# Optimization experiments

Hardware: AMD Instinct MI355X
Metric: run time of the kernel (lower is better)

The kernel has to match this reference:

```python
import math
import jax, jax.numpy as jnp
import numpy as np

NH, NKV, HD = 16, 8, 128  # n_heads, n_kv_heads, head_dim from config

def setup_inputs() -> dict:
    key = jax.random.key(0)
    ks = jax.random.split(key, 5)
    B, T, D = 2, 2048, 2048
    KV = NKV * HD  # 1024
    s = 1.0 / math.sqrt(D)
    return {
        "x": jax.random.normal(ks[0], (B, T, D), dtype=jnp.float32),
        "Wq": jax.random.normal(ks[1], (D, D), dtype=jnp.float32) * s,
        "Wk": jax.random.normal(ks[2], (KV, D), dtype=jnp.float32) * s,
        "Wv": jax.random.normal(ks[3], (KV, D), dtype=jnp.float32) * s,
        "Wo": jax.random.normal(ks[4], (D, D), dtype=jnp.float32) * s,
    }

def reference(x, Wq, Wk, Wv, Wo):
    B, T, D = x.shape
    groups = NH // NKV
    scale = 1.0 / math.sqrt(HD)
    # Projections (torch Linear: y = x @ W.T)
    q = (x @ Wq.T).reshape(B, T, NH, HD).transpose(0, 2, 1, 3)    # [B, nh, T, hd]
    k = (x @ Wk.T).reshape(B, T, NKV, HD).transpose(0, 2, 1, 3)   # [B, nkv, T, hd]
    v = (x @ Wv.T).reshape(B, T, NKV, HD).transpose(0, 2, 1, 3)   # [B, nkv, T, hd]
    kv_state = jnp.concatenate([k, v], axis=-1)                    # [B, nkv, T, 2*hd]
    # GQA: replicate kv heads (repeat_interleave along head dim)
    k = jnp.repeat(k, groups, axis=1)                              # [B, nh, T, hd]
    v = jnp.repeat(v, groups, axis=1)
    scores = jnp.einsum('bhqd,bhkd->bhqk', q, k) * scale           # [B, nh, T, T]
    causal = jnp.tril(jnp.ones((T, T), dtype=bool))
    scores = jnp.where(causal, scores, jnp.finfo(scores.dtype).min)
    probs = jax.nn.softmax(scores, axis=-1)
    attn = jnp.einsum('bhqk,bhkd->bhqd', probs, v)                 # [B, nh, T, hd]
    attn = attn.transpose(0, 2, 1, 3).reshape(B, T, NH * HD)
    output = attn @ Wo.T
    return (output, kv_state)
```

## Files before the change

kernel.cpp:

```cpp
#include <hip/hip_runtime.h>
#include <hip/hip_bf16.h>
#include <cstdint>
#include <cstddef>

#define DEV __device__ __forceinline__

typedef __attribute__((ext_vector_type(8))) short short8;
typedef __attribute__((ext_vector_type(4))) float f32x4;
typedef __attribute__((ext_vector_type(8))) __bf16 bf16x8;

DEV unsigned short f2bf(float f) {
    unsigned u = __builtin_bit_cast(unsigned, f);
    u += 0x7fffu + ((u >> 16) & 1u);
    return (unsigned short)(u >> 16);
}

DEV unsigned short f2bf_hw(float f) {
    return __builtin_bit_cast(unsigned short, (__bf16)f);
}

DEV f32x4 mfma16(short8 a, short8 b, f32x4 c) {
    return __builtin_amdgcn_mfma_f32_16x16x32_bf16(
        __builtin_bit_cast(bf16x8, a), __builtin_bit_cast(bf16x8, b), c, 0, 0, 0);
}

#define GLD_TO_LDS16(g, l)                                                  \
    __builtin_amdgcn_global_load_lds(                                       \
        (const __attribute__((address_space(1))) void*)(g),                 \
        (__attribute__((address_space(3))) void*)(l), 16, 0, 0)

__global__ void cvt_all(const float* __restrict__ x,  const float* __restrict__ wq,
                        const float* __restrict__ wk, const float* __restrict__ wv,
                        const float* __restrict__ wo,
                        unsigned short* __restrict__ xb,  unsigned short* __restrict__ wqb,
                        unsigned short* __restrict__ wkb, unsigned short* __restrict__ wvb,
                        unsigned short* __restrict__ wob) {
    constexpr int NX = 1048576, NQ = 524288, NK = 262144, NV = 262144, NO = 524288;
    constexpr int C1 = NX, C2 = C1 + NQ, C3 = C2 + NK, C4 = C3 + NV, C5 = C4 + NO;
    int i = blockIdx.x * blockDim.x + threadIdx.x;
    int stride = gridDim.x * blockDim.x;
    for (; i < C5; i += stride) {
        const float* s;
        unsigned short* d;
        int j;
        if (i < C1)      { s = x;  d = xb;  j = i; }
        else if (i < C2) { s = wq; d = wqb; j = i - C1; }
        else if (i < C3) { s = wk; d = wkb; j = i - C2; }
        else if (i < C4) { s = wv; d = wvb; j = i - C3; }
        else             { s = wo; d = wob; j = i - C4; }
        const f32x4* sp = (const f32x4*)(s + (size_t)j * 8);
        f32x4 a = sp[0], bq = sp[1];
        short8 o;
        o[0] = (short)f2bf(a[0]);  o[1] = (short)f2bf(a[1]);
        o[2] = (short)f2bf(a[2]);  o[3] = (short)f2bf(a[3]);
        o[4] = (short)f2bf(bq[0]); o[5] = (short)f2bf(bq[1]);
        o[6] = (short)f2bf(bq[2]); o[7] = (short)f2bf(bq[3]);
        *(short8*)(d + (size_t)j * 8) = o;
    }
}

__global__ __launch_bounds__(256) void transpose_v(
    const unsigned short* __restrict__ src, unsigned short* __restrict__ dst) {
    __shared__ __align__(16) unsigned short tile[64 * 64];
    const int t0 = blockIdx.x * 64;
    const int d0 = blockIdx.y * 64;
    const int b  = blockIdx.z;
    const int tid = threadIdx.x;
#pragma unroll
    for (int p = 0; p < 2; ++p) {
        int ch = tid + p * 256;
        int it = ch >> 3, ic8 = ch & 7;
        short8 v = *(const short8*)(src + (size_t)(b * 2048 + t0 + it) * 1024 + d0 + ic8 * 8);
        *(short8*)&tile[it * 64 + ((ic8 ^ (it & 7)) << 3)] = v;
    }
    __syncthreads();
#pragma unroll
    for (int p = 0; p < 2; ++p) {
        int ch = tid + p * 256;
        int od = ch >> 3, ot8 = ch & 7;
        short8 v;
#pragma unroll
        for (int j = 0; j < 8; ++j) {
            int t = ot8 * 8 + j;
            v[j] = (short)tile[t * 64 + ((((od >> 3) ^ (t & 7)) << 3) | (od & 7))];
        }
        *(short8*)(dst + (size_t)(b * 1024 + d0 + od) * 2048 + t0 + ot8 * 8) = v;
    }
}

__global__ __launch_bounds__(512, 2) void gemm_qkv_8p(
    const unsigned short* __restrict__ A,
    const unsigned short* __restrict__ Wq, const unsigned short* __restrict__ Wk,
    const unsigned short* __restrict__ Wv,
    unsigned short* __restrict__ Qo, unsigned short* __restrict__ Ko,
    unsigned short* __restrict__ Vo, float* __restrict__ kvf) {
    constexpr int K = 2048, BM = 256, KT = K / 64;
    __shared__ __align__(16) unsigned short sA[2][2][BM][32];
    __shared__ __align__(16) unsigned short sB[2][2][BM][32];

    const int tid = threadIdx.x, lane = tid & 63, w = tid >> 6;
    const int wm = w >> 2, wn = w & 3;
    const int lrow = lane & 15, lg = lane >> 4;
    const int m0 = blockIdx.y * BM, n0 = blockIdx.x * BM;

    const unsigned short* Bp;
    unsigned short* Co;
    int c0, ostr, doff = 0;
    bool iskv = false;
    if (n0 < 2048)      { Bp = Wq + (size_t)n0 * K;        Co = Qo; c0 = n0;        ostr = 2048; }
    else if (n0 < 3072) { Bp = Wk + (size_t)(n0-2048) * K; Co = Ko; c0 = n0 - 2048; ostr = 1024; iskv = true; }
    else                { Bp = Wv + (size_t)(n0-3072) * K; Co = Vo; c0 = n0 - 3072; ostr = 1024; iskv = true; doff = 128; }

    const unsigned short* Ab = A + (size_t)m0 * K;

    auto stage = [&](const unsigned short* gcol, unsigned short* lds) {
#pragma unroll
        for (int p = 0; p < 2; ++p) {
            int ch = tid + p * 512;
            int row = ch >> 2;
            int slot = (ch & 3) ^ (row & 3);
            GLD_TO_LDS16(gcol + (size_t)row * K + slot * 8, lds + ch * 8);
        }
    };

    f32x4 acc[8][4];
#pragma unroll
    for (int i = 0; i < 8; ++i)
#pragma unroll
        for (int j = 0; j < 4; ++j) acc[i][j] = (f32x4)0.f;

    const int xoff = (lg * 8) ^ ((lrow & 3) << 3);
    const int arow0 = wm * 128 + lrow;
    const int brow0 = wn * 64 + lrow;
    short8 afrag[4], bfrag[4];

    stage(Ab,      &sA[0][0][0][0]);
    stage(Bp,      &sB[0][0][0][0]);
    stage(Ab + 32, &sA[0][1][0][0]);
    stage(Bp + 32, &sB[0][1][0][0]);
    asm volatile("s_waitcnt vmcnt(4)\n\ts_barrier" ::: "memory");

#define PHASE(BUF, NB, KS, MQ, DOSTAGE, VM)                                        \
    do {                                                                           \
        if ((MQ) == 0) {                                                           \
            _Pragma("unroll")                                                      \
            for (int ni = 0; ni < 4; ++ni)                                         \
                bfrag[ni] = *(const short8*)(&sB[BUF][KS][brow0 + ni * 16][0] + xoff); \
        }                                                                          \
        _Pragma("unroll")                                                          \
        for (int mi = 0; mi < 4; ++mi)                                             \
            afrag[mi] = *(const short8*)(&sA[BUF][KS][arow0 + (MQ) * 64 + mi * 16][0] + xoff); \
        if (DOSTAGE) {                                                             \
            if ((MQ) == 0) stage(An + (KS) * 32, &sA[NB][KS][0][0]);               \
            else           stage(Bn + (KS) * 32, &sB[NB][KS][0][0]);               \
        }                                                                          \
        asm volatile("s_barrier" ::: "memory");                                    \
        asm volatile("s_waitcnt lgkmcnt(0)" ::: "memory");                         \
        __builtin_amdgcn_sched_barrier(0);                                         \
        __builtin_amdgcn_s_setprio(1);                                             \
        _Pragma("unroll")                                                          \
        for (int mi = 0; mi < 4; ++mi)                                             \
            _Pragma("unroll")                                                      \
            for (int ni = 0; ni < 4; ++ni)                                         \
                acc[(MQ) * 4 + mi][ni] = mfma16(afrag[mi], bfrag[ni], acc[(MQ) * 4 + mi][ni]); \
        __builtin_amdgcn_s_setprio(0);                                             \
        if ((VM) == 4)      asm volatile("s_waitcnt vmcnt(4)" ::: "memory");       \
        else if ((VM) == 0) asm volatile("s_waitcnt vmcnt(0)" ::: "memory");       \
        asm volatile("s_barrier" ::: "memory");                                    \
    } while (0)

    for (int kt = 0; kt < KT; ++kt) {
        const int buf = kt & 1, nb = buf ^ 1;
        const bool pre = (kt + 1 < KT);
        const unsigned short* An = Ab + (kt + 1) * 64;
        const unsigned short* Bn = Bp + (kt + 1) * 64;
        PHASE(buf, nb, 0, 0, pre, -1);
        PHASE(buf, nb, 0, 1, pre, pre ? 4 : 0);
        PHASE(buf, nb, 1, 0, pre, -1);
        PHASE(buf, nb, 1, 1, pre, pre ? 4 : -1);
    }
#undef PHASE

    const int lrow4 = (lane >> 4) * 4, lcol = lane & 15;
#pragma unroll
    for (int mi = 0; mi < 8; ++mi) {
#pragma unroll
        for (int ni = 0; ni < 4; ++ni) {
#pragma unroll
            for (int r = 0; r < 4; ++r) {
                int row = m0 + wm * 128 + mi * 16 + lrow4 + r;
                int col = c0 + wn * 64 + ni * 16 + lcol;
                float v = acc[mi][ni][r];
                Co[(size_t)row * ostr + col] = f2bf(v);
                if (iskv) {
                    int b = row >> 11, t = row & 2047;
                    int kh = col >> 7, d = col & 127;
                    kvf[((size_t)(b * 8 + kh) * 2048 + t) * 256 + doff + d] = v;
                }
            }
        }
    }
}

__global__ __launch_bounds__(256) void gemm_bt_f32(
    const unsigned short* __restrict__ A, const unsigned short* __restrict__ Bm,
    float* __restrict__ Cf, int M, int N, int K) {
    constexpr int BM = 128, BN = 128, BK = 32;
    __shared__ __align__(16) unsigned short sA[2][BM * BK];
    __shared__ __align__(16) unsigned short sB[2][BN * BK];

    const int tid = threadIdx.x;
    const int lane = tid & 63;
    const int wid = tid >> 6;
    const int wr = wid >> 1, wc = wid & 1;
    const int m0 = blockIdx.y * BM, n0 = blockIdx.x * BN;
    const int KT = K / BK;

    auto stage = [&](int buf, int kt) {
#pragma unroll
        for (int p = 0; p < 2; ++p) {
            int ch = tid + p * 256;
            int r = ch >> 2, c = (ch & 3) * 8;
            GLD_TO_LDS16(A + (size_t)(m0 + r) * K + kt * BK + c, &sA[buf][ch * 8]);
        }
#pragma unroll
        for (int p = 0; p < 2; ++p) {
            int ch = tid + p * 256;
            int r = ch >> 2, c = (ch & 3) * 8;
            GLD_TO_LDS16(Bm + (size_t)(n0 + r) * K + kt * BK + c, &sB[buf][ch * 8]);
        }
    };

    f32x4 acc[4][4];
#pragma unroll
    for (int i = 0; i < 4; ++i)
#pragma unroll
        for (int j = 0; j < 4; ++j) acc[i][j] = (f32x4)0.f;

    stage(0, 0);
    int cur = 0;
    const int lrow = lane & 15, lko = (lane >> 4) * 8;
    for (int kt = 0; kt < KT; ++kt) {
        __syncthreads();
        if (kt + 1 < KT) stage(cur ^ 1, kt + 1);
        short8 af[4], bfr[4];
#pragma unroll
        for (int mi = 0; mi < 4; ++mi)
            af[mi] = *(const short8*)&sA[cur][(wr * 64 + mi * 16 + lrow) * BK + lko];
#pragma unroll
        for (int ni = 0; ni < 4; ++ni)
            bfr[ni] = *(const short8*)&sB[cur][(wc * 64 + ni * 16 + lrow) * BK + lko];
#pragma unroll
        for (int mi = 0; mi < 4; ++mi)
#pragma unroll
            for (int ni = 0; ni < 4; ++ni)
                acc[mi][ni] = mfma16(af[mi], bfr[ni], acc[mi][ni]);
        cur ^= 1;
    }

    const int lrow4 = (lane >> 4) * 4, lcol = lane & 15;
#pragma unroll
    for (int mi = 0; mi < 4; ++mi)
#pragma unroll
        for (int ni = 0; ni < 4; ++ni)
#pragma unroll
            for (int r = 0; r < 4; ++r) {
                int row = m0 + wr * 64 + mi * 16 + lrow4 + r;
                int col = n0 + wc * 64 + ni * 16 + lcol;
                Cf[(size_t)row * N + col] = acc[mi][ni][r];
            }
}

__global__ __launch_bounds__(512, 4) void attn_fwd(
    const unsigned short* __restrict__ Qb, const unsigned short* __restrict__ Kb,
    const unsigned short* __restrict__ Vtg, unsigned short* __restrict__ Ob) {
    constexpr int T = 2048, DQ = 2048, DKV = 1024, HD = 128;
    constexpr float SC2 = 0.08838834764831845f * 1.4426950408889634f;
    constexpr float SHIFT = 8.0f * 1.4426950408889634f;
    __shared__ __align__(16) unsigned short Ks[64 * 136];
    __shared__ __align__(16) unsigned short Vs[128 * 72];
    __shared__ __align__(16) unsigned short Ps[8][16 * 72];

    const int bx = blockIdx.x, kh = blockIdx.y, b = blockIdx.z;
    const int qtile = b ? (31 - bx) : bx;
    const int tid = threadIdx.x, lane = tid & 63, w = tid >> 6;
    const int h = kh * 2 + (w >> 2);
    const int lrow = lane & 15, lg = lane >> 4;
    const int qt0 = qtile * 64;
    const int qrow0 = qt0 + (w & 3) * 16;
    const size_t bT = (size_t)b * T;

    short8 qf[4];
    {
        const unsigned short* qbase = Qb + (bT + qrow0 + lrow) * DQ + h * HD + lg * 8;
#pragma unroll
        for (int kc = 0; kc < 4; ++kc) qf[kc] = *(const short8*)(qbase + kc * 32);
    }

    int kr[2], kc8[2], vd[2], vk8[2];
#pragma unroll
    for (int p = 0; p < 2; ++p) {
        int ch = tid + p * 512;
        kr[p] = ch >> 4;  kc8[p] = ch & 15;
        vd[p] = ch >> 3;  vk8[p] = ch & 7;
    }
    const unsigned short* kbase = Kb + bT * DKV + kh * HD;
    const unsigned short* vbase = Vtg + (size_t)(b * 8 + kh) * 128 * T;
    short8 kreg[2], vreg[2];
    auto gload = [&](int kt) {
#pragma unroll
        for (int p = 0; p < 2; ++p) {
            kreg[p] = *(const short8*)(kbase + (size_t)(kt * 64 + kr[p]) * DKV + kc8[p] * 8);
            vreg[p] = *(const short8*)(vbase + (size_t)vd[p] * T + kt * 64 + vk8[p] * 8);
        }
    };
    auto lwrite = [&]() {
#pragma unroll
        for (int p = 0; p < 2; ++p) {
            *(short8*)&Ks[kr[p] * 136 + kc8[p] * 8] = kreg[p];
            *(short8*)&Vs[vd[p] * 72 + vk8[p] * 8] = vreg[p];
        }
    };

    f32x4 o[8];
#pragma unroll
    for (int i = 0; i < 8; ++i) o[i] = (f32x4)0.f;
    float rsum[4] = {0.f, 0.f, 0.f, 0.f};

    const int nkt = qtile + 1;
    gload(0);
    for (int kt = 0; kt < nkt; ++kt) {
        const int kt0 = kt * 64;
        __syncthreads();
        lwrite();
        __syncthreads();
        if (kt + 1 < nkt) gload(kt + 1);

        f32x4 s[4];
        __builtin_amdgcn_s_setprio(1);
#pragma unroll
        for (int nt = 0; nt < 4; ++nt) {
            s[nt] = (f32x4)0.f;
#pragma unroll
            for (int kc = 0; kc < 4; ++kc) {
                short8 kf = *(const short8*)&Ks[(nt * 16 + lrow) * 136 + kc * 32 + lg * 8];
                s[nt] = mfma16(qf[kc], kf, s[nt]);
            }
        }
        __builtin_amdgcn_s_setprio(0);

        const int qabs = qrow0 + lg * 4;
        const bool diag = (kt == qtile);
#pragma unroll
        for (int nt = 0; nt < 4; ++nt) {
            int kcol = kt0 + nt * 16 + lrow;
#pragma unroll
            for (int r = 0; r < 4; ++r) {
                float p = exp2f(fmaf(s[nt][r], SC2, -SHIFT));
                if (diag && kcol > qabs + r) p = 0.f;
                rsum[r] += p;
                Ps[w][(lg * 4 + r) * 72 + nt * 16 + lrow] = f2bf_hw(p);
            }
        }

        __builtin_amdgcn_s_setprio(1);
#pragma unroll
        for (int kc2 = 0; kc2 < 2; ++kc2) {
            short8 pf = *(const short8*)&Ps[w][lrow * 72 + kc2 * 32 + lg * 8];
#pragma unroll
            for (int dt = 0; dt < 8; ++dt) {
                short8 vf = *(const short8*)&Vs[(dt * 16 + lrow) * 72 + kc2 * 32 + lg * 8];
                o[dt] = mfma16(pf, vf, o[dt]);
            }
        }
        __builtin_amdgcn_s_setprio(0);
    }

#pragma unroll
    for (int r = 0; r < 4; ++r) {
        float v = rsum[r];
        v += __shfl_xor(v, 1);
        v += __shfl_xor(v, 2);
        v += __shfl_xor(v, 4);
        v += __shfl_xor(v, 8);
        float inv = 1.f / v;
        int row = qrow0 + lg * 4 + r;
        unsigned short* obase = Ob + (bT + row) * DQ + h * HD + lrow;
#pragma unroll
        for (int dt = 0; dt < 8; ++dt) obase[dt * 16] = f2bf_hw(o[dt][r] * inv);
    }
}

extern "C" void kernel_launch(void* const* d_in, const int* in_sizes, int n_in,
                              void* d_out, int out_size, void* d_ws, size_t ws_size,
                              hipStream_t stream) {
    (void)in_sizes; (void)n_in; (void)out_size; (void)ws_size;
    const float* x  = (const float*)d_in[0];
    const float* Wq = (const float*)d_in[1];
    const float* Wk = (const float*)d_in[2];
    const float* Wv = (const float*)d_in[3];
    const float* Wo = (const float*)d_in[4];
    float* out = (float*)d_out;
    float* kv_out = out + (size_t)8388608;

    unsigned short* xb   = (unsigned short*)d_ws;
    unsigned short* wqb  = xb   + 8388608;
    unsigned short* wkb  = wqb  + 4194304;
    unsigned short* wvb  = wkb  + 2097152;
    unsigned short* wob  = wvb  + 2097152;
    unsigned short* qb   = wob  + 4194304;
    unsigned short* kb   = qb   + 8388608;
    unsigned short* vt   = kb   + 4194304;
    unsigned short* ab   = vt   + 4194304;
    unsigned short* vtmp = ab;

    cvt_all<<<dim3(2048), dim3(256), 0, stream>>>(x, Wq, Wk, Wv, Wo,
                                                  xb, wqb, wkb, wvb, wob);
    gemm_qkv_8p<<<dim3(16, 16), 512, 0, stream>>>(xb, wqb, wkb, wvb, qb, kb, vtmp, kv_out);
    transpose_v<<<dim3(32, 16, 2), 256, 0, stream>>>(vtmp, vt);
    attn_fwd<<<dim3(32, 8, 2), 512, 0, stream>>>(qb, kb, vt, ab);
    gemm_bt_f32<<<dim3(16, 32), 256, 0, stream>>>(ab, wob, out, 4096, 2048, 2048);
}
```

Baseline: 237.7 us.

## Rewrite output projection GEMM with 256x128 tiles, swizzled LDS, split-K pipelining

Replaces the 128x128, 256-thread output-projection GEMM with a 512-thread kernel that computes 256x128 tiles. Each 64-wide K step is split into two 32-wide halves, and the next tile is prefetched one half at a time with fine-grained vmcnt waits. LDS rows are XOR-swizzled to avoid bank conflicts, and the MFMA blocks run at raised priority. The aim is more data reuse per block, better overlap of loads with compute, and fewer LDS conflicts. It also drops a sched_barrier in the QKV GEMM phase, which lets the compiler reorder code there.

After: 242.0 us. Within noise of the previous version (+1.8%).

```diff
diff --git a/kernel.cpp b/kernel.cpp
--- a/kernel.cpp
+++ b/kernel.cpp
@@ -156,7 +156,6 @@
         }                                                                          \
         asm volatile("s_barrier" ::: "memory");                                    \
         asm volatile("s_waitcnt lgkmcnt(0)" ::: "memory");                         \
-        __builtin_amdgcn_sched_barrier(0);                                         \
         __builtin_amdgcn_s_setprio(1);                                             \
         _Pragma("unroll")                                                          \
         for (int mi = 0; mi < 4; ++mi)                                             \
@@ -202,34 +201,36 @@
     }
 }
 
-__global__ __launch_bounds__(256) void gemm_bt_f32(
+__global__ __launch_bounds__(512, 2) void gemm_o_2p(
     const unsigned short* __restrict__ A, const unsigned short* __restrict__ Bm,
-    float* __restrict__ Cf, int M, int N, int K) {
-    constexpr int BM = 128, BN = 128, BK = 32;
-    __shared__ __align__(16) unsigned short sA[2][BM * BK];
-    __shared__ __align__(16) unsigned short sB[2][BN * BK];
-
-    const int tid = threadIdx.x;
-    const int lane = tid & 63;
-    const int wid = tid >> 6;
-    const int wr = wid >> 1, wc = wid & 1;
-    const int m0 = blockIdx.y * BM, n0 = blockIdx.x * BN;
-    const int KT = K / BK;
-
-    auto stage = [&](int buf, int kt) {
+    float* __restrict__ Cf) {
+    constexpr int K = 2048, N = 2048, KT = K / 64;
+    __shared__ __align__(16) unsigned short sA[2][2][256][32];
+    __shared__ __align__(16) unsigned short sB[2][2][128][32];
+
+    const int tid = threadIdx.x, lane = tid & 63, w = tid >> 6;
+    const int wm = w >> 1, wn = w & 1;
+    const int lrow = lane & 15, lg = lane >> 4;
+    const int m0 = blockIdx.y * 256, n0 = blockIdx.x * 128;
+
+    const unsigned short* Ab = A + (size_t)m0 * K;
+    const unsigned short* Bb = Bm + (size_t)n0 * K;
+
+    auto stageA = [&](const unsigned short* gcol, unsigned short* lds) {
 #pragma unroll
         for (int p = 0; p < 2; ++p) {
-            int ch = tid + p * 256;
-            int r = ch >> 2, c = (ch & 3) * 8;
-            GLD_TO_LDS16(A + (size_t)(m0 + r) * K + kt * BK + c, &sA[buf][ch * 8]);
-        }
-#pragma unroll
-        for (int p = 0; p < 2; ++p) {
-            int ch = tid + p * 256;
-            int r = ch >> 2, c = (ch & 3) * 8;
-            GLD_TO_LDS16(Bm + (size_t)(n0 + r) * K + kt * BK + c, &sB[buf][ch * 8]);
+            int ch = tid + p * 512;
+            int row = ch >> 2;
+            int slot = (ch & 3) ^ (row & 3);
+            GLD_TO_LDS16(gcol + (size_t)row * K + slot * 8, lds + ch * 8);
         }
     };
+    auto stageB = [&](const unsigned short* gcol, unsigned short* lds) {
+        int ch = tid;
+        int row = ch >> 2;
+        int slot = (ch & 3) ^ (row & 3);
+        GLD_TO_LDS16(gcol + (size_t)row * K + slot * 8, lds + ch * 8);
+    };
 
     f32x4 acc[4][4];
 #pragma unroll
@@ -237,25 +238,57 @@
 #pragma unroll
         for (int j = 0; j < 4; ++j) acc[i][j] = (f32x4)0.f;
 
-    stage(0, 0);
-    int cur = 0;
-    const int lrow = lane & 15, lko = (lane >> 4) * 8;
+    const int xoff = (lg * 8) ^ ((lrow & 3) << 3);
+    const int arow0 = wm * 64 + lrow;
+    const int brow0 = wn * 64 + lrow;
+
+    stageA(Ab,      &sA[0][0][0][0]);
+    stageB(Bb,      &sB[0][0][0][0]);
+    stageA(Ab + 32, &sA[0][1][0][0]);
+    stageB(Bb + 32, &sB[0][1][0][0]);
+    asm volatile("s_waitcnt vmcnt(3)\n\ts_barrier" ::: "memory");
+
     for (int kt = 0; kt < KT; ++kt) {
-        __syncthreads();
-        if (kt + 1 < KT) stage(cur ^ 1, kt + 1);
-        short8 af[4], bfr[4];
+        const int buf = kt & 1, nb = buf ^ 1;
+        const bool pre = (kt + 1 < KT);
+        const unsigned short* An = Ab + (kt + 1) * 64;
+        const unsigned short* Bn = Bb + (kt + 1) * 64;
+        short8 afrag[4], bfrag[4];
+
+        if (pre) { stageA(An, &sA[nb][0][0][0]); stageB(Bn, &sB[nb][0][0][0]); }
+#pragma unroll
+        for (int ni = 0; ni < 4; ++ni)
+            bfrag[ni] = *(const short8*)(&sB[buf][0][brow0 + ni * 16][0] + xoff);
 #pragma unroll
         for (int mi = 0; mi < 4; ++mi)
-            af[mi] = *(const short8*)&sA[cur][(wr * 64 + mi * 16 + lrow) * BK + lko];
+            afrag[mi] = *(const short8*)(&sA[buf][0][arow0 + mi * 16][0] + xoff);
+        __builtin_amdgcn_s_setprio(1);
+#pragma unroll
+        for (int mi = 0; mi < 4; ++mi)
+#pragma unroll
+            for (int ni = 0; ni < 4; ++ni)
+                acc[mi][ni] = mfma16(afrag[mi], bfrag[ni], acc[mi][ni]);
+        __builtin_amdgcn_s_setprio(0);
+
+        if (pre) asm volatile("s_waitcnt vmcnt(3)\n\ts_barrier" ::: "memory");
+        else     asm volatile("s_waitcnt vmcnt(0)\n\ts_barrier" ::: "memory");
+
+        if (pre) { stageA(An + 32, &sA[nb][1][0][0]); stageB(Bn + 32, &sB[nb][1][0][0]); }
 #pragma unroll
         for (int ni = 0; ni < 4; ++ni)
-            bfr[ni] = *(const short8*)&sB[cur][(wc * 64 + ni * 16 + lrow) * BK + lko];
+            bfrag[ni] = *(const short8*)(&sB[buf][1][brow0 + ni * 16][0] + xoff);
 #pragma unroll
         for (int mi = 0; mi < 4; ++mi)
+            afrag[mi] = *(const short8*)(&sA[buf][1][arow0 + mi * 16][0] + xoff);
+        __builtin_amdgcn_s_setprio(1);
+#pragma unroll
+        for (int mi = 0; mi < 4; ++mi)
 #pragma unroll
             for (int ni = 0; ni < 4; ++ni)
-                acc[mi][ni] = mfma16(af[mi], bfr[ni], acc[mi][ni]);
-        cur ^= 1;
+                acc[mi][ni] = mfma16(afrag[mi], bfrag[ni], acc[mi][ni]);
+        __builtin_amdgcn_s_setprio(0);
+
+        if (pre) asm volatile("s_waitcnt vmcnt(3)\n\ts_barrier" ::: "memory");
     }
 
     const int lrow4 = (lane >> 4) * 4, lcol = lane & 15;
@@ -265,8 +298,8 @@
         for (int ni = 0; ni < 4; ++ni)
 #pragma unroll
             for (int r = 0; r < 4; ++r) {
-                int row = m0 + wr * 64 + mi * 16 + lrow4 + r;
-                int col = n0 + wc * 64 + ni * 16 + lcol;
+                int row = m0 + wm * 64 + mi * 16 + lrow4 + r;
+                int col = n0 + wn * 64 + ni * 16 + lcol;
                 Cf[(size_t)row * N + col] = acc[mi][ni][r];
             }
 }
@@ -419,5 +452,5 @@
     gemm_qkv_8p<<<dim3(16, 16), 512, 0, stream>>>(xb, wqb, wkb, wvb, qb, kb, vtmp, kv_out);
     transpose_v<<<dim3(32, 16, 2), 256, 0, stream>>>(vtmp, vt);
     attn_fwd<<<dim3(32, 8, 2), 512, 0, stream>>>(qb, kb, vt, ab);
-    gemm_bt_f32<<<dim3(16, 32), 256, 0, stream>>>(ab, wob, out, 4096, 2048, 2048);
-}
+    gemm_o_2p<<<dim3(16, 16), 512, 0, stream>>>(ab, wob, out);
+}
```
